# Kernel tuning notes

Hardware: AMD Instinct MI355X
Metric: run time of the kernel (lower is better)

Reference implementation:

```python
import jax, jax.numpy as jnp
import numpy as np
from jax import lax

Z_DIM = 256
X_DIM = 64
SEQ_LEN = 12
BATCH = 8192


def setup_inputs() -> dict:
    key = jax.random.key(0)
    k1, k2, k3, k4 = jax.random.split(key, 4)
    tokens = jax.random.randint(k1, (SEQ_LEN, BATCH), 0, X_DIM, dtype=jnp.int32)
    T_logits = jax.random.normal(k2, (Z_DIM, Z_DIM), dtype=jnp.float32)
    pi_logits = jax.random.normal(k3, (Z_DIM,), dtype=jnp.float32)
    emit_logits = jax.random.normal(k4, (X_DIM, Z_DIM), dtype=jnp.float32)
    return {"tokens": tokens, "T_logits": T_logits, "pi_logits": pi_logits,
            "emit_logits": emit_logits}


def reference(tokens, T_logits, pi_logits, emit_logits):
    # Column-wise softmaxes, matching nn.Softmax(dim=0) in the torch module.
    T = jax.nn.softmax(T_logits, axis=0)        # (Z, Z), columns sum to 1
    pi = jax.nn.softmax(pi_logits, axis=0)      # (Z,)
    emit = jax.nn.softmax(emit_logits, axis=0)  # (X, Z), columns sum to 1

    e = emit[tokens]                            # (S, B, Z) gathered emissions

    # alpha[0] = emit[input[0]] * pi  (only alpha[0] feeds log_marginal)
    alpha0 = e[0] * pi[None, :]                 # (B, Z)

    # Backward recursion: beta[t] = (emit[input[t+1]] * beta[t+1]) @ T
    def bwd_step(b, e_next):
        return (e_next * b) @ T, None

    beta_last = jnp.ones((tokens.shape[1], Z_DIM), dtype=T.dtype)
    beta0, _ = lax.scan(bwd_step, beta_last, e[1:], reverse=True)  # (B, Z)

    # log_marginal = logsumexp(log(alpha0) + log(beta0), axis=-1)
    log_marginal = jax.scipy.special.logsumexp(
        jnp.log(alpha0) + jnp.log(beta0), axis=-1)  # (B,)

    # Module's forward() returns the negative log marginal.
    return -log_marginal
```

## Files before the change

kernel.cpp:

```cpp
#include <hip/hip_runtime.h>
#include <math.h>


#define ZD 256
#define XD 64
#define SL 12
#define BM 32

typedef short bf16x8 __attribute__((ext_vector_type(8)));
typedef float f32x4  __attribute__((ext_vector_type(4)));

#define TP_BYTES   131072
#define BETA_OFF   131072
#define TOK_OFF    147456
#define RED_OFF    148992
#define SMEM_BYTES 150016

__device__ __forceinline__ ushort f2bf(float f) {
    uint u = __float_as_uint(f);
    return (ushort)((u + 0x7FFFu + ((u >> 16) & 1u)) >> 16);
}
__device__ __forceinline__ float bflo(uint w) { return __uint_as_float(w << 16); }
__device__ __forceinline__ float bfhi(uint w) { return __uint_as_float(w & 0xFFFF0000u); }
__device__ __forceinline__ uint pk_bf16(float lo, float hi) {
    uint r;
    asm("v_cvt_pk_bf16_f32 %0, %1, %2" : "=v"(r) : "v"(lo), "v"(hi));
    return r;
}
__device__ __forceinline__ int bswz(int row, int kbyte) {
    return BETA_OFF + row * 512 + (kbyte ^ ((row & 7) << 4));
}

__global__ __launch_bounds__(256) void prep_kernel(
    const float* __restrict__ Tl, const float* __restrict__ pil,
    const float* __restrict__ El, ushort* __restrict__ Tp,
    ushort* __restrict__ emit_g, float* __restrict__ pi_g)
{
    __shared__ float wsum[4];
    const int tid = threadIdx.x;
    const int bid = blockIdx.x;

    if (bid < ZD) {
        const int n = bid, k = tid;
        float e = __expf(Tl[k * ZD + n]);
        float v = e;
        #pragma unroll
        for (int o = 32; o > 0; o >>= 1) v += __shfl_down(v, o);
        if ((tid & 63) == 0) wsum[tid >> 6] = v;
        __syncthreads();
        float inv = 1.f / (wsum[0] + wsum[1] + wsum[2] + wsum[3]);
        int ks = k >> 5, lh = (k >> 3) & 3, j7 = k & 7;
        int ct = n >> 4, ll = n & 15;
        Tp[(((ks * 16 + ct) * 64) + lh * 16 + ll) * 8 + j7] = f2bf(e * inv);
    } else if (bid == ZD) {
        const int z = tid;
        float s = 0.f;
        #pragma unroll 8
        for (int x = 0; x < XD; ++x) s += __expf(El[x * ZD + z]);
        float inv = 1.f / s;
        for (int x = 0; x < XD; ++x)
            emit_g[x * ZD + z] = f2bf(__expf(El[x * ZD + z]) * inv);
    } else {
        float e = __expf(pil[tid]);
        float v = e;
        #pragma unroll
        for (int o = 32; o > 0; o >>= 1) v += __shfl_down(v, o);
        if ((tid & 63) == 0) wsum[tid >> 6] = v;
        __syncthreads();
        pi_g[tid] = e / (wsum[0] + wsum[1] + wsum[2] + wsum[3]);
    }
}

__global__ __launch_bounds__(256) void chain_kernel(
    const int* __restrict__ tokens, const ushort* __restrict__ Tp_g,
    const ushort* __restrict__ emit_g, const float* __restrict__ pi_g,
    float* __restrict__ out, int B)
{
    extern __shared__ __align__(16) char smem[];
    const int tid  = threadIdx.x;
    const int row0 = blockIdx.x * BM;

    {
        const uint4* src = (const uint4*)Tp_g;
        uint4* dst = (uint4*)smem;
        #pragma unroll 8
        for (int i = 0; i < 32; ++i) dst[tid + 256 * i] = src[tid + 256 * i];
    }
    int* toks = (int*)(smem + TOK_OFF);
    for (int i = tid; i < SL * BM; i += 256)
        toks[i] = tokens[(i >> 5) * B + row0 + (i & 31)];
    {
        uint4 one; one.x = one.y = one.z = one.w = 0x3F803F80u;
        #pragma unroll
        for (int c = 0; c < 4; ++c) {
            int g = tid + 256 * c;
            int r = g >> 5, kb = (g & 31) << 4;
            *(uint4*)(smem + bswz(r, kb)) = one;
        }
    }
    __syncthreads();

    const int l  = tid & 63;
    const int w  = tid >> 6;
    const int ll = l & 15;
    const int lh = l >> 4;
    const char* emitb = (const char*)emit_g;

    for (int t = SL - 1; t >= 1; --t) {
        #pragma unroll
        for (int c = 0; c < 4; ++c) {
            int g = tid + 256 * c;
            int r = g >> 5, kb = (g & 31) << 4;
            int tok = toks[t * BM + r];
            char* bp = smem + bswz(r, kb);
            uint4 bb = *(uint4*)bp;
            uint4 ee = *(const uint4*)(emitb + tok * 512 + kb);
            uint4 oo;
            oo.x = pk_bf16(bflo(bb.x) * bflo(ee.x), bfhi(bb.x) * bfhi(ee.x));
            oo.y = pk_bf16(bflo(bb.y) * bflo(ee.y), bfhi(bb.y) * bfhi(ee.y));
            oo.z = pk_bf16(bflo(bb.z) * bflo(ee.z), bfhi(bb.z) * bfhi(ee.z));
            oo.w = pk_bf16(bflo(bb.w) * bflo(ee.w), bfhi(bb.w) * bfhi(ee.w));
            *(uint4*)bp = oo;
        }
        __syncthreads();

        f32x4 acc[2][4];
        #pragma unroll
        for (int rt = 0; rt < 2; ++rt)
            #pragma unroll
            for (int cj = 0; cj < 4; ++cj) acc[rt][cj] = (f32x4)0.f;

        #pragma unroll
        for (int ks = 0; ks < 8; ++ks) {
            bf16x8 af[2], bfr[4];
            #pragma unroll
            for (int rt = 0; rt < 2; ++rt) {
                int r  = rt * 16 + ll;
                int kb = (ks * 32 + lh * 8) * 2;
                af[rt] = *(const bf16x8*)(smem + bswz(r, kb));
            }
            #pragma unroll
            for (int cj = 0; cj < 4; ++cj) {
                int ct = w * 4 + cj;
                bfr[cj] = *(const bf16x8*)(smem + ((ks * 16 + ct) * 64 + l) * 16);
            }
            #pragma unroll
            for (int rt = 0; rt < 2; ++rt)
                #pragma unroll
                for (int cj = 0; cj < 4; ++cj)
                    acc[rt][cj] = __builtin_amdgcn_mfma_f32_16x16x32_bf16(
                        af[rt], bfr[cj], acc[rt][cj], 0, 0, 0);
        }
        __syncthreads();

        #pragma unroll
        for (int rt = 0; rt < 2; ++rt)
            #pragma unroll
            for (int cj = 0; cj < 4; ++cj) {
                int col = (w * 4 + cj) * 16 + ll;
                int r0  = rt * 16 + lh * 4;
                uint w01 = pk_bf16(acc[rt][cj][0], acc[rt][cj][1]);
                uint w23 = pk_bf16(acc[rt][cj][2], acc[rt][cj][3]);
                *(ushort*)(smem + bswz(r0 + 0, col * 2)) = (ushort)w01;
                *(ushort*)(smem + bswz(r0 + 1, col * 2)) = (ushort)(w01 >> 16);
                *(ushort*)(smem + bswz(r0 + 2, col * 2)) = (ushort)w23;
                *(ushort*)(smem + bswz(r0 + 3, col * 2)) = (ushort)(w23 >> 16);
            }
        __syncthreads();
    }

    {
        float* red = (float*)(smem + RED_OFF);
        const int r = tid & 31, q = tid >> 5;
        const int tok0 = toks[r];
        float s = 0.f;
        #pragma unroll
        for (int i = 0; i < 4; ++i) {
            int k0 = q * 32 + i * 8;
            int kb = k0 * 2;
            uint4 bb = *(const uint4*)(smem + bswz(r, kb));
            uint4 ee = *(const uint4*)(emitb + tok0 * 512 + kb);
            const float4* pf = (const float4*)(pi_g + k0);
            float4 pA = pf[0], pB = pf[1];
            s += bflo(bb.x) * bflo(ee.x) * pA.x + bfhi(bb.x) * bfhi(ee.x) * pA.y;
            s += bflo(bb.y) * bflo(ee.y) * pA.z + bfhi(bb.y) * bfhi(ee.y) * pA.w;
            s += bflo(bb.z) * bflo(ee.z) * pB.x + bfhi(bb.z) * bfhi(ee.z) * pB.y;
            s += bflo(bb.w) * bflo(ee.w) * pB.z + bfhi(bb.w) * bfhi(ee.w) * pB.w;
        }
        red[tid] = s;
        __syncthreads();
        if (tid < BM) {
            float tot = 0.f;
            #pragma unroll
            for (int q2 = 0; q2 < 8; ++q2) tot += red[q2 * 32 + tid];
            out[row0 + tid] = -__logf(tot);
        }
    }
}

extern "C" void kernel_launch(void* const* d_in, const int* in_sizes, int n_in,
                              void* d_out, int out_size, void* d_ws, size_t ws_size,
                              hipStream_t stream)
{
    (void)n_in; (void)out_size; (void)ws_size;
    const int*   tokens = (const int*)d_in[0];
    const float* Tl     = (const float*)d_in[1];
    const float* pil    = (const float*)d_in[2];
    const float* El     = (const float*)d_in[3];
    float*       outp   = (float*)d_out;

    const int B = in_sizes[0] / SL;

    char*   wsb    = (char*)d_ws;
    ushort* Tp     = (ushort*)wsb;
    ushort* emit_g = (ushort*)(wsb + TP_BYTES);
    float*  pi_g   = (float*)(wsb + TP_BYTES + 32768);

    hipFuncSetAttribute((const void*)chain_kernel,
                        hipFuncAttributeMaxDynamicSharedMemorySize, SMEM_BYTES);

    prep_kernel<<<ZD + 2, 256, 0, stream>>>(Tl, pil, El, Tp, emit_g, pi_g);
    chain_kernel<<<B / BM, 256, SMEM_BYTES, stream>>>(tokens, Tp, emit_g, pi_g, outp, B);
}
```

Measured before the change: 91.99 us.

## Hold transition matrix in registers, double-buffer beta, fuse emission multiply into MFMA loads

Each wave now loads its slice of the bf16 transition matrix into registers (32 bf16x8 fragments) instead of copying all 128KB into LDS. That cuts LDS use from about 150KB to about 33KB, so several blocks can share a CU, at the cost of many VGPRs. The emission-times-beta product is fused into the A-fragment load of the MFMA loop, reading emissions directly from global/L2. Beta is double-buffered, which removes the separate elementwise pass and two of the three barriers per step. The first step skips the all-ones beta by using the emissions directly.

New measurement: 96.82 us. 5.2% more time.

```diff
diff --git a/kernel.cpp b/kernel.cpp
--- a/kernel.cpp
+++ b/kernel.cpp
@@ -9,12 +9,6 @@
 
 typedef short bf16x8 __attribute__((ext_vector_type(8)));
 typedef float f32x4  __attribute__((ext_vector_type(4)));
-
-#define TP_BYTES   131072
-#define BETA_OFF   131072
-#define TOK_OFF    147456
-#define RED_OFF    148992
-#define SMEM_BYTES 150016
 
 __device__ __forceinline__ ushort f2bf(float f) {
     uint u = __float_as_uint(f);
@@ -28,7 +22,16 @@
     return r;
 }
 __device__ __forceinline__ int bswz(int row, int kbyte) {
-    return BETA_OFF + row * 512 + (kbyte ^ ((row & 7) << 4));
+    return row * 512 + (kbyte ^ ((row & 7) << 4));
+}
+__device__ __forceinline__ bf16x8 bmul(bf16x8 a, bf16x8 b) {
+    union { bf16x8 v; uint4 u; } ua, ub, r;
+    ua.v = a; ub.v = b;
+    r.u.x = pk_bf16(bflo(ua.u.x) * bflo(ub.u.x), bfhi(ua.u.x) * bfhi(ub.u.x));
+    r.u.y = pk_bf16(bflo(ua.u.y) * bflo(ub.u.y), bfhi(ua.u.y) * bfhi(ub.u.y));
+    r.u.z = pk_bf16(bflo(ua.u.z) * bflo(ub.u.z), bfhi(ua.u.z) * bfhi(ub.u.z));
+    r.u.w = pk_bf16(bflo(ua.u.w) * bflo(ub.u.w), bfhi(ua.u.w) * bfhi(ub.u.w));
+    return r.v;
 }
 
 __global__ __launch_bounds__(256) void prep_kernel(
@@ -55,9 +58,10 @@
     } else if (bid == ZD) {
         const int z = tid;
         float s = 0.f;
-        #pragma unroll 8
+        #pragma unroll 16
         for (int x = 0; x < XD; ++x) s += __expf(El[x * ZD + z]);
         float inv = 1.f / s;
+        #pragma unroll 8
         for (int x = 0; x < XD; ++x)
             emit_g[x * ZD + z] = f2bf(__expf(El[x * ZD + z]) * inv);
     } else {
@@ -71,114 +75,106 @@
     }
 }
 
-__global__ __launch_bounds__(256) void chain_kernel(
+template<bool FIRST>
+__device__ __forceinline__ void hmm_step(
+    const char* rbuf, char* wbuf, const int* tokrow, const char* emitb,
+    const bf16x8 (&treg)[4][8], int ll, int lh, int w)
+{
+    f32x4 acc[2][4];
+    #pragma unroll
+    for (int rt = 0; rt < 2; ++rt)
+        #pragma unroll
+        for (int cj = 0; cj < 4; ++cj) acc[rt][cj] = (f32x4)0.f;
+
+    #pragma unroll
+    for (int ks = 0; ks < 8; ++ks) {
+        bf16x8 af[2];
+        #pragma unroll
+        for (int rt = 0; rt < 2; ++rt) {
+            const int r  = rt * 16 + ll;
+            const int kb = (ks * 32 + lh * 8) * 2;
+            const int tok = tokrow[r];
+            bf16x8 ev = *(const bf16x8*)(emitb + tok * 512 + kb);
+            if (FIRST) {
+                af[rt] = ev;
+            } else {
+                bf16x8 bb = *(const bf16x8*)(rbuf + bswz(r, kb));
+                af[rt] = bmul(bb, ev);
+            }
+        }
+        #pragma unroll
+        for (int rt = 0; rt < 2; ++rt)
+            #pragma unroll
+            for (int cj = 0; cj < 4; ++cj)
+                acc[rt][cj] = __builtin_amdgcn_mfma_f32_16x16x32_bf16(
+                    af[rt], treg[cj][ks], acc[rt][cj], 0, 0, 0);
+    }
+
+    #pragma unroll
+    for (int rt = 0; rt < 2; ++rt)
+        #pragma unroll
+        for (int cj = 0; cj < 4; ++cj) {
+            const int col = (w * 4 + cj) * 16 + ll;
+            const int r0  = rt * 16 + lh * 4;
+            uint w01 = pk_bf16(acc[rt][cj][0], acc[rt][cj][1]);
+            uint w23 = pk_bf16(acc[rt][cj][2], acc[rt][cj][3]);
+            *(ushort*)(wbuf + bswz(r0 + 0, col * 2)) = (ushort)w01;
+            *(ushort*)(wbuf + bswz(r0 + 1, col * 2)) = (ushort)(w01 >> 16);
+            *(ushort*)(wbuf + bswz(r0 + 2, col * 2)) = (ushort)w23;
+            *(ushort*)(wbuf + bswz(r0 + 3, col * 2)) = (ushort)(w23 >> 16);
+        }
+}
+
+__global__ __launch_bounds__(256, 1) void chain_kernel(
     const int* __restrict__ tokens, const ushort* __restrict__ Tp_g,
     const ushort* __restrict__ emit_g, const float* __restrict__ pi_g,
     float* __restrict__ out, int B)
 {
-    extern __shared__ __align__(16) char smem[];
+    __shared__ __align__(16) char beta[2][BM * 512];
+    __shared__ int   toks[SL][BM];
+    __shared__ float red[8][BM];
+
     const int tid  = threadIdx.x;
     const int row0 = blockIdx.x * BM;
-
-    {
-        const uint4* src = (const uint4*)Tp_g;
-        uint4* dst = (uint4*)smem;
-        #pragma unroll 8
-        for (int i = 0; i < 32; ++i) dst[tid + 256 * i] = src[tid + 256 * i];
-    }
-    int* toks = (int*)(smem + TOK_OFF);
-    for (int i = tid; i < SL * BM; i += 256)
-        toks[i] = tokens[(i >> 5) * B + row0 + (i & 31)];
-    {
-        uint4 one; one.x = one.y = one.z = one.w = 0x3F803F80u;
-        #pragma unroll
-        for (int c = 0; c < 4; ++c) {
-            int g = tid + 256 * c;
-            int r = g >> 5, kb = (g & 31) << 4;
-            *(uint4*)(smem + bswz(r, kb)) = one;
-        }
-    }
-    __syncthreads();
-
     const int l  = tid & 63;
     const int w  = tid >> 6;
     const int ll = l & 15;
     const int lh = l >> 4;
     const char* emitb = (const char*)emit_g;
 
-    for (int t = SL - 1; t >= 1; --t) {
-        #pragma unroll
-        for (int c = 0; c < 4; ++c) {
-            int g = tid + 256 * c;
-            int r = g >> 5, kb = (g & 31) << 4;
-            int tok = toks[t * BM + r];
-            char* bp = smem + bswz(r, kb);
-            uint4 bb = *(uint4*)bp;
-            uint4 ee = *(const uint4*)(emitb + tok * 512 + kb);
-            uint4 oo;
-            oo.x = pk_bf16(bflo(bb.x) * bflo(ee.x), bfhi(bb.x) * bfhi(ee.x));
-            oo.y = pk_bf16(bflo(bb.y) * bflo(ee.y), bfhi(bb.y) * bfhi(ee.y));
-            oo.z = pk_bf16(bflo(bb.z) * bflo(ee.z), bfhi(bb.z) * bfhi(ee.z));
-            oo.w = pk_bf16(bflo(bb.w) * bflo(ee.w), bfhi(bb.w) * bfhi(ee.w));
-            *(uint4*)bp = oo;
-        }
-        __syncthreads();
-
-        f32x4 acc[2][4];
-        #pragma unroll
-        for (int rt = 0; rt < 2; ++rt)
+    bf16x8 treg[4][8];
+    {
+        const bf16x8* TG = (const bf16x8*)Tp_g;
+        #pragma unroll
+        for (int ks = 0; ks < 8; ++ks)
             #pragma unroll
-            for (int cj = 0; cj < 4; ++cj) acc[rt][cj] = (f32x4)0.f;
-
-        #pragma unroll
-        for (int ks = 0; ks < 8; ++ks) {
-            bf16x8 af[2], bfr[4];
-            #pragma unroll
-            for (int rt = 0; rt < 2; ++rt) {
-                int r  = rt * 16 + ll;
-                int kb = (ks * 32 + lh * 8) * 2;
-                af[rt] = *(const bf16x8*)(smem + bswz(r, kb));
-            }
-            #pragma unroll
-            for (int cj = 0; cj < 4; ++cj) {
-                int ct = w * 4 + cj;
-                bfr[cj] = *(const bf16x8*)(smem + ((ks * 16 + ct) * 64 + l) * 16);
-            }
-            #pragma unroll
-            for (int rt = 0; rt < 2; ++rt)
-                #pragma unroll
-                for (int cj = 0; cj < 4; ++cj)
-                    acc[rt][cj] = __builtin_amdgcn_mfma_f32_16x16x32_bf16(
-                        af[rt], bfr[cj], acc[rt][cj], 0, 0, 0);
-        }
-        __syncthreads();
-
-        #pragma unroll
-        for (int rt = 0; rt < 2; ++rt)
-            #pragma unroll
-            for (int cj = 0; cj < 4; ++cj) {
-                int col = (w * 4 + cj) * 16 + ll;
-                int r0  = rt * 16 + lh * 4;
-                uint w01 = pk_bf16(acc[rt][cj][0], acc[rt][cj][1]);
-                uint w23 = pk_bf16(acc[rt][cj][2], acc[rt][cj][3]);
-                *(ushort*)(smem + bswz(r0 + 0, col * 2)) = (ushort)w01;
-                *(ushort*)(smem + bswz(r0 + 1, col * 2)) = (ushort)(w01 >> 16);
-                *(ushort*)(smem + bswz(r0 + 2, col * 2)) = (ushort)w23;
-                *(ushort*)(smem + bswz(r0 + 3, col * 2)) = (ushort)(w23 >> 16);
-            }
-        __syncthreads();
+            for (int cj = 0; cj < 4; ++cj)
+                treg[cj][ks] = TG[(ks * 16 + (w * 4 + cj)) * 64 + l];
+    }
+
+    for (int i = tid; i < SL * BM; i += 256)
+        toks[i >> 5][i & 31] = tokens[(i >> 5) * B + row0 + (i & 31)];
+    __syncthreads();
+
+    hmm_step<true>(beta[1], beta[0], &toks[SL - 1][0], emitb, treg, ll, lh, w);
+    __syncthreads();
+    int cur = 0;
+    for (int t = SL - 2; t >= 1; --t) {
+        hmm_step<false>(beta[cur], beta[cur ^ 1], &toks[t][0], emitb, treg, ll, lh, w);
+        __syncthreads();
+        cur ^= 1;
     }
 
     {
-        float* red = (float*)(smem + RED_OFF);
+        const char* fb = beta[cur];
         const int r = tid & 31, q = tid >> 5;
-        const int tok0 = toks[r];
+        const int tok0 = toks[0][r];
         float s = 0.f;
         #pragma unroll
         for (int i = 0; i < 4; ++i) {
             int k0 = q * 32 + i * 8;
             int kb = k0 * 2;
-            uint4 bb = *(const uint4*)(smem + bswz(r, kb));
+            uint4 bb = *(const uint4*)(fb + bswz(r, kb));
             uint4 ee = *(const uint4*)(emitb + tok0 * 512 + kb);
             const float4* pf = (const float4*)(pi_g + k0);
             float4 pA = pf[0], pB = pf[1];
@@ -187,12 +183,12 @@
             s += bflo(bb.z) * bflo(ee.z) * pB.x + bfhi(bb.z) * bfhi(ee.z) * pB.y;
             s += bflo(bb.w) * bflo(ee.w) * pB.z + bfhi(bb.w) * bfhi(ee.w) * pB.w;
         }
-        red[tid] = s;
+        red[q][r] = s;
         __syncthreads();
         if (tid < BM) {
             float tot = 0.f;
             #pragma unroll
-            for (int q2 = 0; q2 < 8; ++q2) tot += red[q2 * 32 + tid];
+            for (int q2 = 0; q2 < 8; ++q2) tot += red[q2][tid];
             out[row0 + tid] = -__logf(tot);
         }
     }
@@ -213,12 +209,9 @@
 
     char*   wsb    = (char*)d_ws;
     ushort* Tp     = (ushort*)wsb;
-    ushort* emit_g = (ushort*)(wsb + TP_BYTES);
-    float*  pi_g   = (float*)(wsb + TP_BYTES + 32768);
-
-    hipFuncSetAttribute((const void*)chain_kernel,
-                        hipFuncAttributeMaxDynamicSharedMemorySize, SMEM_BYTES);
+    ushort* emit_g = (ushort*)(wsb + 131072);
+    float*  pi_g   = (float*)(wsb + 131072 + 32768);
 
     prep_kernel<<<ZD + 2, 256, 0, stream>>>(Tl, pil, El, Tp, emit_g, pi_g);
-    chain_kernel<<<B / BM, 256, SMEM_BYTES, stream>>>(tokens, Tp, emit_g, pi_g, outp, B);
-}
+    chain_kernel<<<B / BM, 256, 0, stream>>>(tokens, Tp, emit_g, pi_g, outp, B);
+}
```
